# Kernel optimization log

Hardware: AMD Instinct MI355X
Metric: run time of the kernel (lower is better)

## Reference

```python
import jax, jax.numpy as jnp
import numpy as np

H = 512  # hidden_size


def setup_inputs() -> dict:
    key = jax.random.key(0)
    ks = jax.random.split(key, 7)
    B, T, I = 256, 512, 3
    s = 1.0 / np.sqrt(H)
    return {
        "x": jax.random.normal(ks[0], (B, T, I), dtype=jnp.float32),
        "W_ih": jax.random.uniform(ks[1], (4 * H, I), dtype=jnp.float32, minval=-s, maxval=s),
        "W_hh": jax.random.uniform(ks[2], (4 * H, H), dtype=jnp.float32, minval=-s, maxval=s),
        "b_ih": jax.random.uniform(ks[3], (4 * H,), dtype=jnp.float32, minval=-s, maxval=s),
        "b_hh": jax.random.uniform(ks[4], (4 * H,), dtype=jnp.float32, minval=-s, maxval=s),
        "fc_w": jax.random.uniform(ks[5], (1, H), dtype=jnp.float32, minval=-s, maxval=s),
        "fc_b": jax.random.uniform(ks[6], (1,), dtype=jnp.float32, minval=-s, maxval=s),
    }


def _lstm_last_h(x, W_ih, W_hh, b_ih, b_hh):
    B = x.shape[0]
    # precompute input contribution for all timesteps: [B, T, 4H]
    x_gates = jnp.einsum('bti,gi->btg', x, W_ih) + (b_ih + b_hh)
    h0 = jnp.zeros((B, H), dtype=x.dtype)
    c0 = jnp.zeros((B, H), dtype=x.dtype)

    def step(carry, xg):
        h, c = carry
        gates = xg + h @ W_hh.T  # [B, 4H]
        i, f, g, o = jnp.split(gates, 4, axis=-1)  # torch order: i, f, g, o
        i = jax.nn.sigmoid(i)
        f = jax.nn.sigmoid(f)
        g = jnp.tanh(g)
        o = jax.nn.sigmoid(o)
        c_new = f * c + i * g
        h_new = o * jnp.tanh(c_new)
        return (h_new, c_new), None

    (h_last, _), _ = jax.lax.scan(step, (h0, c0), jnp.swapaxes(x_gates, 0, 1))
    return h_last  # [B, H]


def reference(x, W_ih, W_hh, b_ih, b_hh, fc_w, fc_b):
    h_last = _lstm_last_h(x, W_ih, W_hh, b_ih, b_hh)
    return h_last @ fc_w.T + fc_b  # [B, 1]
```

## Files before the change

### kernel.cpp

```cpp
#include <hip/hip_runtime.h>


#define Hh   512
#define Bsz  256
#define Tt   512

#define MB   16
#define HS   32
#define NROW 128
#define NTHR 512
#define NWG  256

typedef float    f32x4 __attribute__((ext_vector_type(4)));
typedef _Float16 f16x8 __attribute__((ext_vector_type(8)));
typedef unsigned long long u64;

#define PLANE_ELE (Bsz * Hh)
#define PLANES   3
#define BAR_OFF  (PLANES * PLANE_ELE * 2)
#define CTRL_UINTS 4096

__device__ __forceinline__ float sigm(float v)  { return 1.0f / (1.0f + __expf(-v)); }
__device__ __forceinline__ float tanhx(float v) { return 2.0f / (1.0f + __expf(-2.0f * v)) - 1.0f; }

__device__ __forceinline__ float h2f(ushort u) {
  return (float)__builtin_bit_cast(_Float16, u);
}
__device__ __forceinline__ ushort f2h(float f) {
  return __builtin_bit_cast(ushort, (_Float16)f);
}

#define GLOAD(dst, base, imm)                                            \
  asm volatile("global_load_dwordx4 %0, %1, off offset:%c2 sc0 sc1"      \
               : "=v"(dst) : "v"(base), "i"(imm))

__global__ void init_ws(unsigned* ctrl) {
  for (int i = threadIdx.x; i < CTRL_UINTS; i += NTHR) ctrl[i] = 0u;
}

__global__ __launch_bounds__(NTHR, 2)
void lstm_kernel(const float* __restrict__ x,   const float* __restrict__ Wih,
                 const float* __restrict__ Whh, const float* __restrict__ bih,
                 const float* __restrict__ bhh, const float* __restrict__ fcw,
                 const float* __restrict__ fcb, float* __restrict__ out,
                 char* __restrict__ ws)
{
  const int tid = threadIdx.x;
  const int wg  = blockIdx.x;
  const int bb  = wg & 15;
  const int hb  = wg >> 4;
  const int j0  = hb * HS;
  const int b0  = bb * MB;

  ushort*   hpl   = (ushort*)ws;
  unsigned* flags = (unsigned*)(ws + BAR_OFF) + bb * 256;

  __shared__ float gates2[4][NROW][17];
  __shared__ float wih_s[NROW][3];
  __shared__ float bsum[NROW];
  __shared__ float xs[MB][3];

  if (tid < NROW) {
    int qq = tid >> 5, jj = tid & 31;
    int grow = qq * Hh + j0 + jj;
    wih_s[tid][0] = Wih[grow * 3 + 0];
    wih_s[tid][1] = Wih[grow * 3 + 1];
    wih_s[tid][2] = Wih[grow * 3 + 2];
    bsum[tid] = bih[grow] + bhh[grow];
  }

  const int l   = tid & 63;
  const int ks  = tid >> 6;
  const int lm  = l & 15;
  const int lk  = l >> 4;

  f16x8 wfrag[8][2];
  #pragma unroll
  for (int rb = 0; rb < 8; ++rb) {
    #pragma unroll
    for (int kb = 0; kb < 2; ++kb) {
      int rr = rb * 16 + lm;
      int grow = (rr >> 5) * Hh + j0 + (rr & 31);
      int col = (ks * 2 + kb) * 32 + lk * 8;
      const float* wsrc = Whh + (size_t)grow * Hh + col;
      float4 wa = *(const float4*)(wsrc);
      float4 wb = *(const float4*)(wsrc + 4);
      f16x8 f;
      f[0] = (_Float16)wa.x; f[1] = (_Float16)wa.y;
      f[2] = (_Float16)wa.z; f[3] = (_Float16)wa.w;
      f[4] = (_Float16)wb.x; f[5] = (_Float16)wb.y;
      f[6] = (_Float16)wb.z; f[7] = (_Float16)wb.w;
      wfrag[rb][kb] = f;
    }
  }

  {
    int cb0 = tid >> 5, cj0 = tid & 31;
    size_t o = (size_t)(b0 + cb0) * Hh + j0 + cj0;
    __hip_atomic_store(&hpl[o], (ushort)0, __ATOMIC_RELAXED, __HIP_MEMORY_SCOPE_AGENT);
  }
  asm volatile("s_waitcnt vmcnt(0)" ::: "memory");
  __syncthreads();
  if (tid == 0) {
    unsigned fv = 1u;
    asm volatile("global_store_dword %0, %1, off sc0 sc1"
                 :: "v"(flags + hb * 16), "v"(fv) : "memory");
  }

  const size_t aoff = (size_t)(b0 + lm) * Hh + ks * 64 + lk * 8;

  const int cb = tid >> 5;
  const int cj = tid & 31;
  float c_state = 0.0f;

  int rd = 0, wr = 1;
  for (int t = 0; t < Tt; ++t) {
    {
      const unsigned tq = (unsigned)(t + 1);
      const unsigned tw = (unsigned)t;
      if (ks == 0) {
        unsigned v = 0xFFFFFFFFu;
        const unsigned* fp = flags + (l & 15) * 16;
        for (;;) {
          if (l < 16)
            asm volatile("global_load_dword %0, %1, off sc0 sc1" : "=v"(v) : "v"(fp) : "memory");
          asm volatile("s_waitcnt vmcnt(0)" ::: "memory");
          unsigned need = ((l & 15) < 2) ? tq : tw;
          if (__all((int)(v >= need))) break;
          __builtin_amdgcn_s_sleep(2);
        }
      } else {
        unsigned v = 0xFFFFFFFFu;
        const unsigned* fp = flags + (ks * 2 + (l & 1)) * 16;
        for (;;) {
          if (l < 2)
            asm volatile("global_load_dword %0, %1, off sc0 sc1" : "=v"(v) : "v"(fp) : "memory");
          asm volatile("s_waitcnt vmcnt(0)" ::: "memory");
          if (__all((int)(v >= tq))) break;
          __builtin_amdgcn_s_sleep(2);
        }
      }
    }

    if (tid < MB * 3) {
      int b = tid / 3, ii = tid - b * 3;
      xs[b][ii] = x[(size_t)(b0 + b) * (Tt * 3) + t * 3 + ii];
    }

    const char* pH = (const char*)(hpl + (size_t)rd * PLANE_ELE + aoff);
    f32x4 AH[2];
    GLOAD(AH[0], pH, 0);  GLOAD(AH[1], pH, 64);
    asm volatile("s_waitcnt vmcnt(0)" ::: "memory");
    __builtin_amdgcn_sched_barrier(0);

    f32x4 acc[8];
    #pragma unroll
    for (int rb = 0; rb < 8; ++rb) acc[rb] = (f32x4){0.f, 0.f, 0.f, 0.f};
    #pragma unroll
    for (int kb = 0; kb < 2; ++kb) {
      f16x8 ah = __builtin_bit_cast(f16x8, AH[kb]);
      #pragma unroll
      for (int rb = 0; rb < 8; ++rb)
        acc[rb] = __builtin_amdgcn_mfma_f32_16x16x32_f16(ah, wfrag[rb][kb], acc[rb], 0, 0, 0);
    }

    if (ks < 4) {
      #pragma unroll
      for (int rb = 0; rb < 8; ++rb)
        #pragma unroll
        for (int r = 0; r < 4; ++r)
          gates2[ks][rb * 16 + lm][lk * 4 + r] = acc[rb][r];
    }
    __syncthreads();
    if (ks >= 4) {
      #pragma unroll
      for (int rb = 0; rb < 8; ++rb)
        #pragma unroll
        for (int r = 0; r < 4; ++r)
          gates2[ks - 4][rb * 16 + lm][lk * 4 + r] += acc[rb][r];
    }
    __syncthreads();

    {
      float xv0 = xs[cb][0], xv1 = xs[cb][1], xv2 = xs[cb][2];
      float pre[4];
      #pragma unroll
      for (int qq = 0; qq < 4; ++qq) {
        int rrq = qq * 32 + cj;
        pre[qq] = gates2[0][rrq][cb] + gates2[1][rrq][cb]
                + gates2[2][rrq][cb] + gates2[3][rrq][cb] + bsum[rrq]
                + xv0 * wih_s[rrq][0] + xv1 * wih_s[rrq][1] + xv2 * wih_s[rrq][2];
      }
      float ig = sigm(pre[0]), fg = sigm(pre[1]);
      float gg = tanhx(pre[2]), og = sigm(pre[3]);
      c_state = fg * c_state + ig * gg;
      float hv = og * tanhx(c_state);
      unsigned uhw = f2h(hv);
      size_t ho = (size_t)wr * PLANE_ELE + (size_t)(b0 + cb) * Hh + j0 + cj;
      asm volatile("global_store_short %0, %1, off sc0 sc1" :: "v"(hpl + ho), "v"(uhw));
    }

    asm volatile("s_waitcnt vmcnt(0)" ::: "memory");
    __syncthreads();
    if (tid == 0) {
      unsigned fv = (unsigned)(t + 2);
      asm volatile("global_store_dword %0, %1, off sc0 sc1"
                   :: "v"(flags + hb * 16), "v"(fv) : "memory");
    }

    rd = wr;
    wr = (wr == 2) ? 0 : wr + 1;
  }

  if (hb == 0) {
    if (tid < 64) {
      unsigned v = 0xFFFFFFFFu;
      const unsigned* fp = flags + (l & 15) * 16;
      const unsigned tgt = (unsigned)(Tt + 1);
      for (;;) {
        if (l < 16)
          asm volatile("global_load_dword %0, %1, off sc0 sc1" : "=v"(v) : "v"(fp) : "memory");
        asm volatile("s_waitcnt vmcnt(0)" ::: "memory");
        if (__all((int)(v >= tgt))) break;
        __builtin_amdgcn_s_sleep(2);
      }
    }
    __syncthreads();

    const u64* Hf = (const u64*)(hpl + (size_t)rd * PLANE_ELE);
    int b = tid >> 5, lj = tid & 31;
    float p = 0.0f;
    for (int jq = lj; jq < Hh / 4; jq += 32) {
      size_t o = (size_t)(b0 + b) * (Hh / 4) + jq;
      u64 uh = __hip_atomic_load(Hf + o, __ATOMIC_RELAXED, __HIP_MEMORY_SCOPE_AGENT);
      #pragma unroll
      for (int e = 0; e < 4; ++e)
        p += h2f((ushort)(uh >> (16 * e))) * fcw[4 * jq + e];
    }
    __syncthreads();
    ((float*)gates2)[tid] = p;
    __syncthreads();
    if (lj == 0) {
      float s = 0.0f;
      #pragma unroll
      for (int r = 0; r < 32; ++r) s += ((float*)gates2)[(b << 5) + r];
      out[b0 + b] = s + fcb[0];
    }
  }
}

extern "C" void kernel_launch(void* const* d_in, const int* in_sizes, int n_in,
                              void* d_out, int out_size, void* d_ws, size_t ws_size,
                              hipStream_t stream) {
  const float* x   = (const float*)d_in[0];
  const float* Wih = (const float*)d_in[1];
  const float* Whh = (const float*)d_in[2];
  const float* bih = (const float*)d_in[3];
  const float* bhh = (const float*)d_in[4];
  const float* fcw = (const float*)d_in[5];
  const float* fcb = (const float*)d_in[6];
  float* out = (float*)d_out;
  char*  ws  = (char*)d_ws;

  hipLaunchKernelGGL(init_ws, dim3(1), dim3(NTHR), 0, stream,
                     (unsigned*)(ws + BAR_OFF));
  hipLaunchKernelGGL(lstm_kernel, dim3(NWG), dim3(NTHR), 0, stream,
                     x, Wih, Whh, bih, bhh, fcw, fcb, out, ws);
}
```

Before: 1.698 ms.

## Embed step tags in hidden-state words to replace flag-based barriers

Each hidden value is now stored as a 32-bit word with the timestep tag in the upper half and fp16 h in the lower half. Consumers spin directly on the h data until every tag matches, which replaces the per-step flag poll and the end-of-step store drain, syncthreads and flag store. A separate progress flag, written right after the gate reduction, is kept only to guard the 3-plane ring against write-after-read reuse. In exchange, h traffic doubles, the A-fragment load grows from two to four dwordx4 loads and needs repacking, and the spin loops gain iteration caps that could silently break out early.

```diff
diff --git a/kernel.cpp b/kernel.cpp
--- a/kernel.cpp
+++ b/kernel.cpp
@@ -12,13 +12,14 @@
 #define NWG  256
 
 typedef float    f32x4 __attribute__((ext_vector_type(4)));
+typedef unsigned u32x4 __attribute__((ext_vector_type(4)));
 typedef _Float16 f16x8 __attribute__((ext_vector_type(8)));
 typedef unsigned long long u64;
 
 #define PLANE_ELE (Bsz * Hh)
 #define PLANES   3
-#define BAR_OFF  (PLANES * PLANE_ELE * 2)
-#define CTRL_UINTS 4096
+#define BAR_OFF  (PLANES * PLANE_ELE * 4)
+#define CTRL_UINTS 8192
 
 __device__ __forceinline__ float sigm(float v)  { return 1.0f / (1.0f + __expf(-v)); }
 __device__ __forceinline__ float tanhx(float v) { return 2.0f / (1.0f + __expf(-2.0f * v)) - 1.0f; }
@@ -52,10 +53,10 @@
   const int j0  = hb * HS;
   const int b0  = bb * MB;
 
-  ushort*   hpl   = (ushort*)ws;
-  unsigned* flags = (unsigned*)(ws + BAR_OFF) + bb * 256;
-
-  __shared__ float gates2[4][NROW][17];
+  unsigned* hpl  = (unsigned*)ws;
+  unsigned* ctrl = (unsigned*)(ws + BAR_OFF) + bb * 512;
+
+  __shared__ float gates2[4][NROW][20];
   __shared__ float wih_s[NROW][3];
   __shared__ float bsum[NROW];
   __shared__ float xs[MB][3];
@@ -97,14 +98,8 @@
   {
     int cb0 = tid >> 5, cj0 = tid & 31;
     size_t o = (size_t)(b0 + cb0) * Hh + j0 + cj0;
-    __hip_atomic_store(&hpl[o], (ushort)0, __ATOMIC_RELAXED, __HIP_MEMORY_SCOPE_AGENT);
-  }
-  asm volatile("s_waitcnt vmcnt(0)" ::: "memory");
-  __syncthreads();
-  if (tid == 0) {
-    unsigned fv = 1u;
-    asm volatile("global_store_dword %0, %1, off sc0 sc1"
-                 :: "v"(flags + hb * 16), "v"(fv) : "memory");
+    unsigned v0 = 0x00010000u;
+    asm volatile("global_store_dword %0, %1, off sc0 sc1" :: "v"(hpl + o), "v"(v0));
   }
 
   const size_t aoff = (size_t)(b0 + lm) * Hh + ks * 64 + lk * 8;
@@ -115,53 +110,74 @@
 
   int rd = 0, wr = 1;
   for (int t = 0; t < Tt; ++t) {
-    {
-      const unsigned tq = (unsigned)(t + 1);
-      const unsigned tw = (unsigned)t;
-      if (ks == 0) {
+    if (tid < MB * 3) {
+      int b = tid / 3, ii = tid - b * 3;
+      xs[b][ii] = x[(size_t)(b0 + b) * (Tt * 3) + t * 3 + ii];
+    }
+
+    if (ks == 0) {
+      const unsigned twar = (t >= 1) ? (unsigned)(t - 1) : 0u;
+      if (twar > 0) {
         unsigned v = 0xFFFFFFFFu;
-        const unsigned* fp = flags + (l & 15) * 16;
+        const unsigned* fp = ctrl + (l & 15) * 16;
+        int spins = 0;
         for (;;) {
           if (l < 16)
             asm volatile("global_load_dword %0, %1, off sc0 sc1" : "=v"(v) : "v"(fp) : "memory");
           asm volatile("s_waitcnt vmcnt(0)" ::: "memory");
-          unsigned need = ((l & 15) < 2) ? tq : tw;
-          if (__all((int)(v >= need))) break;
-          __builtin_amdgcn_s_sleep(2);
+          if (__all((int)(v >= twar))) break;
+          if (++spins > (1 << 16)) break;
+          __builtin_amdgcn_s_sleep(1);
         }
-      } else {
-        unsigned v = 0xFFFFFFFFu;
-        const unsigned* fp = flags + (ks * 2 + (l & 1)) * 16;
-        for (;;) {
-          if (l < 2)
-            asm volatile("global_load_dword %0, %1, off sc0 sc1" : "=v"(v) : "v"(fp) : "memory");
-          asm volatile("s_waitcnt vmcnt(0)" ::: "memory");
-          if (__all((int)(v >= tq))) break;
-          __builtin_amdgcn_s_sleep(2);
+      }
+    }
+
+    const char* pA = (const char*)(hpl + (size_t)rd * PLANE_ELE + aoff);
+    const unsigned exp_hi = ((unsigned)(t + 1)) << 16;
+    u32x4 D0, D1, D2, D3;
+    {
+      int spins = 0;
+      for (;;) {
+        GLOAD(D0, pA, 0);   GLOAD(D1, pA, 16);
+        GLOAD(D2, pA, 128); GLOAD(D3, pA, 144);
+        asm volatile("s_waitcnt vmcnt(0)" ::: "memory");
+        unsigned bad = 0;
+        #pragma unroll
+        for (int e = 0; e < 4; ++e) {
+          bad |= (D0[e] ^ exp_hi) & 0xFFFF0000u;
+          bad |= (D1[e] ^ exp_hi) & 0xFFFF0000u;
+          bad |= (D2[e] ^ exp_hi) & 0xFFFF0000u;
+          bad |= (D3[e] ^ exp_hi) & 0xFFFF0000u;
         }
-      }
-    }
-
-    if (tid < MB * 3) {
-      int b = tid / 3, ii = tid - b * 3;
-      xs[b][ii] = x[(size_t)(b0 + b) * (Tt * 3) + t * 3 + ii];
-    }
-
-    const char* pH = (const char*)(hpl + (size_t)rd * PLANE_ELE + aoff);
-    f32x4 AH[2];
-    GLOAD(AH[0], pH, 0);  GLOAD(AH[1], pH, 64);
-    asm volatile("s_waitcnt vmcnt(0)" ::: "memory");
+        if (__all((int)(bad == 0u))) break;
+        if (++spins > (1 << 16)) break;
+        __builtin_amdgcn_s_sleep(1);
+      }
+    }
     __builtin_amdgcn_sched_barrier(0);
+
+    f16x8 ahk[2];
+    {
+      ushort tmp0[8], tmp1[8];
+      #pragma unroll
+      for (int e = 0; e < 4; ++e) {
+        tmp0[e]     = (ushort)(D0[e] & 0xFFFFu);
+        tmp0[e + 4] = (ushort)(D1[e] & 0xFFFFu);
+        tmp1[e]     = (ushort)(D2[e] & 0xFFFFu);
+        tmp1[e + 4] = (ushort)(D3[e] & 0xFFFFu);
+      }
+      ahk[0] = __builtin_bit_cast(f16x8, *(u32x4*)tmp0);
+      ahk[1] = __builtin_bit_cast(f16x8, *(u32x4*)tmp1);
+    }
 
     f32x4 acc[8];
     #pragma unroll
     for (int rb = 0; rb < 8; ++rb) acc[rb] = (f32x4){0.f, 0.f, 0.f, 0.f};
     #pragma unroll
     for (int kb = 0; kb < 2; ++kb) {
-      f16x8 ah = __builtin_bit_cast(f16x8, AH[kb]);
       #pragma unroll
       for (int rb = 0; rb < 8; ++rb)
-        acc[rb] = __builtin_amdgcn_mfma_f32_16x16x32_f16(ah, wfrag[rb][kb], acc[rb], 0, 0, 0);
+        acc[rb] = __builtin_amdgcn_mfma_f32_16x16x32_f16(ahk[kb], wfrag[rb][kb], acc[rb], 0, 0, 0);
     }
 
     if (ks < 4) {
@@ -172,6 +188,11 @@
           gates2[ks][rb * 16 + lm][lk * 4 + r] = acc[rb][r];
     }
     __syncthreads();
+    if (tid == 0) {
+      unsigned pv = (unsigned)(t + 1);
+      asm volatile("global_store_dword %0, %1, off sc0 sc1"
+                   :: "v"(ctrl + hb * 16), "v"(pv) : "memory");
+    }
     if (ks >= 4) {
       #pragma unroll
       for (int rb = 0; rb < 8; ++rb)
@@ -195,34 +216,35 @@
       float gg = tanhx(pre[2]), og = sigm(pre[3]);
       c_state = fg * c_state + ig * gg;
       float hv = og * tanhx(c_state);
-      unsigned uhw = f2h(hv);
+      unsigned uw = ((unsigned)(t + 2) << 16) | (unsigned)f2h(hv);
       size_t ho = (size_t)wr * PLANE_ELE + (size_t)(b0 + cb) * Hh + j0 + cj;
-      asm volatile("global_store_short %0, %1, off sc0 sc1" :: "v"(hpl + ho), "v"(uhw));
-    }
-
-    asm volatile("s_waitcnt vmcnt(0)" ::: "memory");
-    __syncthreads();
-    if (tid == 0) {
-      unsigned fv = (unsigned)(t + 2);
-      asm volatile("global_store_dword %0, %1, off sc0 sc1"
-                   :: "v"(flags + hb * 16), "v"(fv) : "memory");
+      asm volatile("global_store_dword %0, %1, off sc0 sc1" :: "v"(hpl + ho), "v"(uw));
     }
 
     rd = wr;
     wr = (wr == 2) ? 0 : wr + 1;
+  }
+
+  asm volatile("s_waitcnt vmcnt(0)" ::: "memory");
+  __syncthreads();
+  if (tid == 0) {
+    unsigned dv = 1u;
+    asm volatile("global_store_dword %0, %1, off sc0 sc1"
+                 :: "v"(ctrl + 256 + hb * 16), "v"(dv) : "memory");
   }
 
   if (hb == 0) {
     if (tid < 64) {
       unsigned v = 0xFFFFFFFFu;
-      const unsigned* fp = flags + (l & 15) * 16;
-      const unsigned tgt = (unsigned)(Tt + 1);
+      const unsigned* fp = ctrl + 256 + (l & 15) * 16;
+      int spins = 0;
       for (;;) {
         if (l < 16)
           asm volatile("global_load_dword %0, %1, off sc0 sc1" : "=v"(v) : "v"(fp) : "memory");
         asm volatile("s_waitcnt vmcnt(0)" ::: "memory");
-        if (__all((int)(v >= tgt))) break;
-        __builtin_amdgcn_s_sleep(2);
+        if (__all((int)(v >= 1u))) break;
+        if (++spins > (1 << 16)) break;
+        __builtin_amdgcn_s_sleep(1);
       }
     }
     __syncthreads();
@@ -230,12 +252,11 @@
     const u64* Hf = (const u64*)(hpl + (size_t)rd * PLANE_ELE);
     int b = tid >> 5, lj = tid & 31;
     float p = 0.0f;
-    for (int jq = lj; jq < Hh / 4; jq += 32) {
-      size_t o = (size_t)(b0 + b) * (Hh / 4) + jq;
+    for (int jd = lj; jd < Hh / 2; jd += 32) {
+      size_t o = (size_t)(b0 + b) * (Hh / 2) + jd;
       u64 uh = __hip_atomic_load(Hf + o, __ATOMIC_RELAXED, __HIP_MEMORY_SCOPE_AGENT);
-      #pragma unroll
-      for (int e = 0; e < 4; ++e)
-        p += h2f((ushort)(uh >> (16 * e))) * fcw[4 * jq + e];
+      p += h2f((ushort)(uh & 0xFFFFu)) * fcw[2 * jd];
+      p += h2f((ushort)((uh >> 32) & 0xFFFFu)) * fcw[2 * jd + 1];
     }
     __syncthreads();
     ((float*)gates2)[tid] = p;
```

After: 2.289 ms. 34.8% more time.
